# Optimization experiments

Measured on AMD Instinct MI355X. Metric: run time of the kernel, lower is better.

## Reference

```python
import jax, jax.numpy as jnp
import numpy as np

N = 100000   # nodes
E = 1600000  # edges
IN = 128
H = 128
OUT = 128
G = 1000     # graphs


def setup_inputs() -> dict:
    key = jax.random.key(0)
    ks = jax.random.split(key, 6)
    x = jax.random.normal(ks[0], (N, IN), jnp.float32)
    edge_index = jax.random.randint(ks[1], (2, E), 0, N, dtype=jnp.int64)
    batch = jnp.sort(jax.random.randint(ks[2], (N,), 0, G, dtype=jnp.int64))
    # Glorot-ish init for the two GCN linear transforms
    W1 = jax.random.normal(ks[3], (IN, H), jnp.float32) * (1.0 / np.sqrt(IN))
    b1 = jnp.zeros((H,), jnp.float32)
    W2 = jax.random.normal(ks[4], (H, OUT), jnp.float32) * (1.0 / np.sqrt(H))
    b2 = jnp.zeros((OUT,), jnp.float32)
    return {"x": x, "edge_index": edge_index, "batch": batch,
            "W1": W1, "b1": b1, "W2": W2, "b2": b2, "num_graphs": G}


def reference(x, edge_index, batch, W1, b1, W2, b2, num_graphs):
    n = x.shape[0]
    src, dst = edge_index[0], edge_index[1]
    # GCN normalization with self-loops: deg includes the self-loop (+1)
    deg = jax.ops.segment_sum(jnp.ones(src.shape[0], x.dtype), dst,
                              num_segments=n) + 1.0
    dinv = jax.lax.rsqrt(deg)                 # [N]
    norm = dinv[src] * dinv[dst]              # [E] per-edge coefficient
    self_norm = dinv * dinv                   # [N] self-loop coefficient

    def gcn_conv(h, W, b):
        hw = h @ W                                            # [N, F] dense transform
        msg = norm[:, None] * hw[src]                         # gather + scale, [E, F]
        agg = jax.ops.segment_sum(msg, dst, num_segments=n)   # scatter-add
        return agg + self_norm[:, None] * hw + b              # self-loop + bias

    h = jax.nn.relu(gcn_conv(x, W1, b1))
    h = gcn_conv(h, W2, b2)

    # global_mean_pool over graph ids
    sums = jax.ops.segment_sum(h, batch, num_segments=num_graphs)
    counts = jax.ops.segment_sum(jnp.ones(n, h.dtype), batch,
                                 num_segments=num_graphs)
    return sums / jnp.maximum(counts, 1.0)[:, None]
```

## Files before the change

### kernel.cpp

```cpp
#include <hip/hip_runtime.h>
#include <hip/hip_fp16.h>

#define FDIM 128
#define BROWS 64
#define KCH 16
#define NCH (FDIM / KCH)
#define BSHIFT 9
#define BNODES 512
#define EPB 4096


__global__ __launch_bounds__(256) void bucket_count(const int* __restrict__ dst,
                                                    int* __restrict__ bcnt, int E) {
    __shared__ int lc[256];
    lc[threadIdx.x] = 0;
    __syncthreads();
    for (int e = blockIdx.x * blockDim.x + threadIdx.x; e < E;
         e += gridDim.x * blockDim.x)
        atomicAdd(&lc[dst[e] >> BSHIFT], 1);
    __syncthreads();
    int c = lc[threadIdx.x];
    if (c) atomicAdd(&bcnt[threadIdx.x], c);
}

__global__ void bucket_scan(const int* __restrict__ bcnt, int* __restrict__ bbase,
                            int* __restrict__ bcur, int* __restrict__ rp,
                            int E, int n, int nbuck) {
    __shared__ int s[2][256];
    int t = threadIdx.x;
    int v = (t < nbuck) ? bcnt[t] : 0;
    s[0][t] = v;
    __syncthreads();
    int cur = 0;
    for (int off = 1; off < 256; off <<= 1) {
        int x = s[cur][t];
        if (t >= off) x += s[cur][t - off];
        s[cur ^ 1][t] = x;
        cur ^= 1;
        __syncthreads();
    }
    int ex = s[cur][t] - v;
    if (t < nbuck) { bbase[t] = ex; bcur[t] = ex; }
    if (t == 0) { bbase[nbuck] = E; rp[n] = E; }
}

__global__ __launch_bounds__(256) void binscatter(const int* __restrict__ src,
                                                  const int* __restrict__ dst,
                                                  int* __restrict__ bcur,
                                                  int2* __restrict__ eb, int E) {
    __shared__ int lcnt[256];
    __shared__ int gb[256];
    const int t = threadIdx.x;
    const int e0 = blockIdx.x * EPB;
    const int e1 = min(e0 + EPB, E);
    lcnt[t] = 0;
    __syncthreads();
    for (int e = e0 + t; e < e1; e += 256)
        atomicAdd(&lcnt[dst[e] >> BSHIFT], 1);
    __syncthreads();
    int c = lcnt[t];
    if (c) gb[t] = atomicAdd(&bcur[t], c);
    __syncthreads();
    lcnt[t] = 0;
    __syncthreads();
    for (int e = e0 + t; e < e1; e += 256) {
        int d = dst[e];
        int b = d >> BSHIFT;
        int lo = atomicAdd(&lcnt[b], 1);
        eb[gb[b] + lo] = make_int2(src[e], d);
    }
}

__global__ __launch_bounds__(256) void csr_count(const int2* __restrict__ eb,
                                                 const int* __restrict__ bbase,
                                                 int* __restrict__ rp,
                                                 float* __restrict__ dinv, int n) {
    __shared__ int lcnt[BNODES];
    __shared__ int s[2][BNODES];
    const int t = threadIdx.x;
    const int node0 = blockIdx.x << BSHIFT;
    const int nloc = min(BNODES, n - node0);
    lcnt[t] = 0; lcnt[t + 256] = 0;
    __syncthreads();
    const int eb0 = bbase[blockIdx.x], eb1 = bbase[blockIdx.x + 1];
    for (int e = eb0 + t; e < eb1; e += 256)
        atomicAdd(&lcnt[eb[e].y - node0], 1);
    __syncthreads();
    s[0][t] = lcnt[t]; s[0][t + 256] = lcnt[t + 256];
    __syncthreads();
    int cur = 0;
    for (int off = 1; off < BNODES; off <<= 1) {
        int x0 = s[cur][t];       if (t >= off)        x0 += s[cur][t - off];
        int x1 = s[cur][t + 256]; if (t + 256 >= off)  x1 += s[cur][t + 256 - off];
        s[cur ^ 1][t] = x0; s[cur ^ 1][t + 256] = x1;
        cur ^= 1;
        __syncthreads();
    }
    if (t < nloc) {
        rp[node0 + t] = eb0 + s[cur][t] - lcnt[t];
        dinv[node0 + t] = rsqrtf((float)lcnt[t] + 1.0f);
    }
    if (t + 256 < nloc) {
        rp[node0 + t + 256] = eb0 + s[cur][t + 256] - lcnt[t + 256];
        dinv[node0 + t + 256] = rsqrtf((float)lcnt[t + 256] + 1.0f);
    }
}

__global__ __launch_bounds__(256) void csr_fill(const int2* __restrict__ eb,
                                                const int* __restrict__ bbase,
                                                const int* __restrict__ rp,
                                                const float* __restrict__ dinv,
                                                int2* __restrict__ em, int n) {
    __shared__ int lcur[BNODES];
    const int t = threadIdx.x;
    const int node0 = blockIdx.x << BSHIFT;
    const int nloc = min(BNODES, n - node0);
    if (t < nloc) lcur[t] = rp[node0 + t];
    if (t + 256 < nloc) lcur[t + 256] = rp[node0 + t + 256];
    __syncthreads();
    const int eb0 = bbase[blockIdx.x], eb1 = bbase[blockIdx.x + 1];
    for (int e = eb0 + t; e < eb1; e += 256) {
        int2 sd = eb[e];
        int pos = atomicAdd(&lcur[sd.y - node0], 1);
        em[pos] = make_int2(sd.x, __float_as_int(dinv[sd.x] * dinv[sd.y]));
    }
}

__global__ void graph_counts(const int* __restrict__ batch, int* __restrict__ gcnt, int n) {
    int i = blockIdx.x * blockDim.x + threadIdx.x;
    if (i < n) atomicAdd(&gcnt[batch[i]], 1);
}

__global__ __launch_bounds__(256) void gemm128(const float* __restrict__ X,
                                               const float* __restrict__ W,
                                               __half* __restrict__ Y, int n) {
    __shared__ float Ws[FDIM * FDIM];
    __shared__ float xs[2][BROWS][KCH + 4];

    const int tid  = threadIdx.x;
    const int c    = tid & 15;
    const int r    = tid >> 4;
    const int srow = tid >> 2;
    const int skk  = (tid & 3) << 2;
    const int r0   = blockIdx.x * BROWS;

    for (int i = tid; i < FDIM * FDIM; i += 256) Ws[i] = W[i];

    const int grow  = r0 + srow;
    const bool rowok = grow < n;
    const float* xrow = X + (size_t)grow * FDIM + skk;

    float4 v = rowok ? *(const float4*)xrow : float4{0.f, 0.f, 0.f, 0.f};
    *(float4*)&xs[0][srow][skk] = v;
    __syncthreads();

    float accA[4][4], accB[4][4];
#pragma unroll
    for (int m = 0; m < 4; ++m)
#pragma unroll
        for (int i = 0; i < 4; ++i) { accA[m][i] = 0.f; accB[m][i] = 0.f; }

    for (int ch = 0; ch < NCH; ++ch) {
        const int b = ch & 1;
        float4 nv{0.f, 0.f, 0.f, 0.f};
        if (ch + 1 < NCH && rowok)
            nv = *(const float4*)(xrow + (ch + 1) * KCH);
        const int k0 = ch * KCH;
#pragma unroll
        for (int k4 = 0; k4 < KCH; k4 += 4) {
            float4 xv0 = *(const float4*)&xs[b][r][k4];
            float4 xv1 = *(const float4*)&xs[b][r + 16][k4];
            float4 xv2 = *(const float4*)&xs[b][r + 32][k4];
            float4 xv3 = *(const float4*)&xs[b][r + 48][k4];
#define GSTEP(kk, comp)                                                        \
            {                                                                  \
                const float* wp = &Ws[(k0 + k4 + kk) * FDIM + 4 * c];          \
                const float4 w0 = *(const float4*)wp;                          \
                const float4 w1 = *(const float4*)(wp + 64);                   \
                const float xr[4] = {xv0.comp, xv1.comp, xv2.comp, xv3.comp};  \
                _Pragma("unroll")                                              \
                for (int m = 0; m < 4; ++m) {                                  \
                    accA[m][0] = fmaf(xr[m], w0.x, accA[m][0]);                \
                    accA[m][1] = fmaf(xr[m], w0.y, accA[m][1]);                \
                    accA[m][2] = fmaf(xr[m], w0.z, accA[m][2]);                \
                    accB[m][0] = fmaf(xr[m], w1.x, accB[m][0]);                \
                    accB[m][1] = fmaf(xr[m], w1.y, accB[m][1]);                \
                    accB[m][2] = fmaf(xr[m], w1.z, accB[m][2]);                \
                    accB[m][3] = fmaf(xr[m], w1.w, accB[m][3]);                \
                    accA[m][3] = fmaf(xr[m], w0.w, accA[m][3]);                \
                }                                                              \
            }
            GSTEP(0, x) GSTEP(1, y) GSTEP(2, z) GSTEP(3, w)
#undef GSTEP
        }
        if (ch + 1 < NCH)
            *(float4*)&xs[b ^ 1][srow][skk] = nv;
        __syncthreads();
    }

#pragma unroll
    for (int m = 0; m < 4; ++m) {
        int row = r0 + r + 16 * m;
        if (row < n) {
            union { __half2 h[2]; uint2 u; } pa, pb;
            pa.h[0] = __floats2half2_rn(accA[m][0], accA[m][1]);
            pa.h[1] = __floats2half2_rn(accA[m][2], accA[m][3]);
            pb.h[0] = __floats2half2_rn(accB[m][0], accB[m][1]);
            pb.h[1] = __floats2half2_rn(accB[m][2], accB[m][3]);
            *(uint2*)&Y[(size_t)row * FDIM + 4 * c]      = pa.u;
            *(uint2*)&Y[(size_t)row * FDIM + 64 + 4 * c] = pb.u;
        }
    }
}

__device__ __forceinline__ void acc_edge(float4& a, uint2 v, float w) {
    __half2* h = (__half2*)&v;
    float2 f0 = __half22float2(h[0]);
    float2 f1 = __half22float2(h[1]);
    a.x = fmaf(w, f0.x, a.x);
    a.y = fmaf(w, f0.y, a.y);
    a.z = fmaf(w, f1.x, a.z);
    a.w = fmaf(w, f1.y, a.w);
}

__global__ __launch_bounds__(256) void aggregate_relu(
        const __half* __restrict__ hw, const int* __restrict__ rp,
        const int2* __restrict__ em, const float* __restrict__ dinv,
        const float* __restrict__ bias, float* __restrict__ out, int n) {
    const int lane = threadIdx.x & 31;
    const int node = blockIdx.x * 8 + (threadIdx.x >> 5);
    if (node >= n) return;
    const uint2* hw2 = (const uint2*)hw;
    int e0 = rp[node], e1 = rp[node + 1];
    float4 a{0.f, 0.f, 0.f, 0.f};
    int e = e0;
    for (; e + 8 <= e1; e += 8) {
        int2 m[8];
        uint2 v[8];
#pragma unroll
        for (int k = 0; k < 8; ++k) m[k] = em[e + k];
#pragma unroll
        for (int k = 0; k < 8; ++k) v[k] = hw2[(size_t)m[k].x * 32 + lane];
#pragma unroll
        for (int k = 0; k < 8; ++k) acc_edge(a, v[k], __int_as_float(m[k].y));
    }
    for (; e < e1; ++e) {
        int2 m = em[e];
        acc_edge(a, hw2[(size_t)m.x * 32 + lane], __int_as_float(m.y));
    }
    float dv = dinv[node];
    float sn = dv * dv;
    uint2 sv = hw2[(size_t)node * 32 + lane];
    __half2* sh = (__half2*)&sv;
    float2 s0 = __half22float2(sh[0]);
    float2 s1 = __half22float2(sh[1]);
    float4 b = ((const float4*)bias)[lane];
    a.x = fmaxf(fmaf(sn, s0.x, a.x) + b.x, 0.f);
    a.y = fmaxf(fmaf(sn, s0.y, a.y) + b.y, 0.f);
    a.z = fmaxf(fmaf(sn, s1.x, a.z) + b.z, 0.f);
    a.w = fmaxf(fmaf(sn, s1.y, a.w) + b.w, 0.f);
    ((float4*)out)[(size_t)node * 32 + lane] = a;
}

__global__ __launch_bounds__(256) void aggregate_pool(
        const __half* __restrict__ hw, const int* __restrict__ rp,
        const int2* __restrict__ em, const float* __restrict__ dinv,
        const float* __restrict__ bias, const int* __restrict__ batch,
        float* __restrict__ pool, int n) {
    __shared__ float4 part[8][32];
    __shared__ int gs[8];
    const int lane = threadIdx.x & 31;
    const int half = threadIdx.x >> 5;
    const int node = blockIdx.x * 8 + half;
    const bool valid = node < n;
    const uint2* hw2 = (const uint2*)hw;
    int e0 = 0, e1 = 0;
    if (valid) { e0 = rp[node]; e1 = rp[node + 1]; }
    float4 a{0.f, 0.f, 0.f, 0.f};
    int e = e0;
    for (; e + 8 <= e1; e += 8) {
        int2 m[8];
        uint2 v[8];
#pragma unroll
        for (int k = 0; k < 8; ++k) m[k] = em[e + k];
#pragma unroll
        for (int k = 0; k < 8; ++k) v[k] = hw2[(size_t)m[k].x * 32 + lane];
#pragma unroll
        for (int k = 0; k < 8; ++k) acc_edge(a, v[k], __int_as_float(m[k].y));
    }
    for (; e < e1; ++e) {
        int2 m = em[e];
        acc_edge(a, hw2[(size_t)m.x * 32 + lane], __int_as_float(m.y));
    }
    if (valid) {
        float dv = dinv[node];
        float sn = dv * dv;
        uint2 sv = hw2[(size_t)node * 32 + lane];
        __half2* sh = (__half2*)&sv;
        float2 s0 = __half22float2(sh[0]);
        float2 s1 = __half22float2(sh[1]);
        float4 b = ((const float4*)bias)[lane];
        a.x = fmaf(sn, s0.x, a.x) + b.x;
        a.y = fmaf(sn, s0.y, a.y) + b.y;
        a.z = fmaf(sn, s1.x, a.z) + b.z;
        a.w = fmaf(sn, s1.y, a.w) + b.w;
    }
    part[half][lane] = a;
    if (lane == 0) gs[half] = valid ? batch[node] : -1;
    __syncthreads();
    if (half == 0) {
        float4 acc = part[0][lane];
        int g0 = gs[0];
#pragma unroll
        for (int h = 1; h < 8; ++h) {
            if (gs[h] == g0) {
                float4 p = part[h][lane];
                acc.x += p.x; acc.y += p.y; acc.z += p.z; acc.w += p.w;
            } else {
                if (g0 >= 0) {
                    float* dst = &pool[g0 * FDIM + lane * 4];
                    atomicAdd(dst + 0, acc.x); atomicAdd(dst + 1, acc.y);
                    atomicAdd(dst + 2, acc.z); atomicAdd(dst + 3, acc.w);
                }
                g0 = gs[h];
                acc = part[h][lane];
            }
        }
        if (g0 >= 0) {
            float* dst = &pool[g0 * FDIM + lane * 4];
            atomicAdd(dst + 0, acc.x); atomicAdd(dst + 1, acc.y);
            atomicAdd(dst + 2, acc.z); atomicAdd(dst + 3, acc.w);
        }
    }
}

__global__ void pool_div(float* __restrict__ out, const int* __restrict__ gcnt, int total) {
    int i = blockIdx.x * blockDim.x + threadIdx.x;
    if (i < total) {
        int g = i >> 7;
        out[i] /= fmaxf((float)gcnt[g], 1.0f);
    }
}


extern "C" void kernel_launch(void* const* d_in, const int* in_sizes, int n_in,
                              void* d_out, int out_size, void* d_ws, size_t ws_size,
                              hipStream_t stream) {
    const float* x     = (const float*)d_in[0];
    const int*   ei    = (const int*)d_in[1];
    const int*   batch = (const int*)d_in[2];
    const float* W1    = (const float*)d_in[3];
    const float* b1    = (const float*)d_in[4];
    const float* W2    = (const float*)d_in[5];
    const float* b2    = (const float*)d_in[6];
    float* out = (float*)d_out;

    const int N = in_sizes[0] / FDIM;
    const int E = in_sizes[1] / 2;
    const int G = out_size / FDIM;
    const int* src = ei;
    const int* dst = ei + E;
    const int nbuck = (N + BNODES - 1) >> BSHIFT;

    char* p = (char*)d_ws;
    auto alloc = [&](size_t bytes) {
        void* r = (void*)p;
        p += (bytes + 255) & ~(size_t)255;
        return r;
    };
    float*  dinv  = (float*) alloc((size_t)N * 4);
    int*    rp    = (int*)   alloc((size_t)(N + 1) * 4);
    int*    gcnt  = (int*)   alloc((size_t)G * 4);
    int*    bcnt  = (int*)   alloc(256 * 4);
    int*    bbase = (int*)   alloc(257 * 4);
    int*    bcur  = (int*)   alloc(256 * 4);
    int2*   eb    = (int2*)  alloc((size_t)E * 8);
    int2*   em    = (int2*)  alloc((size_t)E * 8);
    __half* hw    = (__half*)alloc((size_t)N * FDIM * 2);
    float*  h1    = (float*) alloc((size_t)N * FDIM * 4);

    hipMemsetAsync(bcnt, 0, 256 * 4, stream);
    hipMemsetAsync(gcnt, 0, (size_t)G * 4, stream);
    hipMemsetAsync(out, 0, (size_t)G * FDIM * 4, stream);

    bucket_count<<<1024, 256, 0, stream>>>(dst, bcnt, E);
    bucket_scan<<<1, 256, 0, stream>>>(bcnt, bbase, bcur, rp, E, N, nbuck);
    binscatter<<<(E + EPB - 1) / EPB, 256, 0, stream>>>(src, dst, bcur, eb, E);
    csr_count<<<nbuck, 256, 0, stream>>>(eb, bbase, rp, dinv, N);
    csr_fill<<<nbuck, 256, 0, stream>>>(eb, bbase, rp, dinv, em, N);
    graph_counts<<<(N + 255) / 256, 256, 0, stream>>>(batch, gcnt, N);

    const int GB = (N + BROWS - 1) / BROWS;
    gemm128<<<GB, 256, 0, stream>>>(x, W1, hw, N);
    aggregate_relu<<<(N + 7) / 8, 256, 0, stream>>>(hw, rp, em, dinv, b1, h1, N);
    gemm128<<<GB, 256, 0, stream>>>(h1, W2, hw, N);
    aggregate_pool<<<(N + 7) / 8, 256, 0, stream>>>(hw, rp, em, dinv, b2, batch, out, N);
    pool_div<<<(G * FDIM + 255) / 256, 256, 0, stream>>>(out, gcnt, G * FDIM);
}
```

Before: 473.4 us.

## Move second GCN linear transform after mean pooling and store h1 in fp16

Uses linearity to reorder the second layer: it aggregates and pools the first-layer activations first, then applies W2 and the bias once per graph in a small pooled GEMM. This removes the full N×128×128 second GEMM and its fp16 intermediate write and read. The relu output h1 is now stored as fp16, which halves its write and its gathered reads but adds rounding error before the second aggregation. The bias is applied only to graphs with nonzero counts, matching mean-pool semantics.

```diff
diff --git a/kernel.cpp b/kernel.cpp
--- a/kernel.cpp
+++ b/kernel.cpp
@@ -226,7 +226,7 @@
 __global__ __launch_bounds__(256) void aggregate_relu(
         const __half* __restrict__ hw, const int* __restrict__ rp,
         const int2* __restrict__ em, const float* __restrict__ dinv,
-        const float* __restrict__ bias, float* __restrict__ out, int n) {
+        const float* __restrict__ bias, __half* __restrict__ out, int n) {
     const int lane = threadIdx.x & 31;
     const int node = blockIdx.x * 8 + (threadIdx.x >> 5);
     if (node >= n) return;
@@ -259,21 +259,23 @@
     a.y = fmaxf(fmaf(sn, s0.y, a.y) + b.y, 0.f);
     a.z = fmaxf(fmaf(sn, s1.x, a.z) + b.z, 0.f);
     a.w = fmaxf(fmaf(sn, s1.y, a.w) + b.w, 0.f);
-    ((float4*)out)[(size_t)node * 32 + lane] = a;
+    union { __half2 h[2]; uint2 u; } pk;
+    pk.h[0] = __floats2half2_rn(a.x, a.y);
+    pk.h[1] = __floats2half2_rn(a.z, a.w);
+    ((uint2*)out)[(size_t)node * 32 + lane] = pk.u;
 }
 
 __global__ __launch_bounds__(256) void aggregate_pool(
-        const __half* __restrict__ hw, const int* __restrict__ rp,
+        const __half* __restrict__ h1, const int* __restrict__ rp,
         const int2* __restrict__ em, const float* __restrict__ dinv,
-        const float* __restrict__ bias, const int* __restrict__ batch,
-        float* __restrict__ pool, int n) {
+        const int* __restrict__ batch, float* __restrict__ pool, int n) {
     __shared__ float4 part[8][32];
     __shared__ int gs[8];
     const int lane = threadIdx.x & 31;
     const int half = threadIdx.x >> 5;
     const int node = blockIdx.x * 8 + half;
     const bool valid = node < n;
-    const uint2* hw2 = (const uint2*)hw;
+    const uint2* hw2 = (const uint2*)h1;
     int e0 = 0, e1 = 0;
     if (valid) { e0 = rp[node]; e1 = rp[node + 1]; }
     float4 a{0.f, 0.f, 0.f, 0.f};
@@ -299,11 +301,10 @@
         __half2* sh = (__half2*)&sv;
         float2 s0 = __half22float2(sh[0]);
         float2 s1 = __half22float2(sh[1]);
-        float4 b = ((const float4*)bias)[lane];
-        a.x = fmaf(sn, s0.x, a.x) + b.x;
-        a.y = fmaf(sn, s0.y, a.y) + b.y;
-        a.z = fmaf(sn, s1.x, a.z) + b.z;
-        a.w = fmaf(sn, s1.y, a.w) + b.w;
+        a.x = fmaf(sn, s0.x, a.x);
+        a.y = fmaf(sn, s0.y, a.y);
+        a.z = fmaf(sn, s1.x, a.z);
+        a.w = fmaf(sn, s1.y, a.w);
     }
     part[half][lane] = a;
     if (lane == 0) gs[half] = valid ? batch[node] : -1;
@@ -334,11 +335,33 @@
     }
 }
 
-__global__ void pool_div(float* __restrict__ out, const int* __restrict__ gcnt, int total) {
-    int i = blockIdx.x * blockDim.x + threadIdx.x;
-    if (i < total) {
-        int g = i >> 7;
-        out[i] /= fmaxf((float)gcnt[g], 1.0f);
+__global__ __launch_bounds__(256) void pool_gemm(const float* __restrict__ pool,
+                                                 const int* __restrict__ gcnt,
+                                                 const float* __restrict__ W2,
+                                                 const float* __restrict__ b2,
+                                                 float* __restrict__ out, int G) {
+    __shared__ float Ws[FDIM * FDIM];
+    __shared__ float row[2][FDIM];
+    for (int i = threadIdx.x; i < FDIM * FDIM; i += 256) Ws[i] = W2[i];
+    const int j  = threadIdx.x & 127;
+    const int gh = threadIdx.x >> 7;
+    for (int g0 = blockIdx.x * 2; g0 < G; g0 += gridDim.x * 2) {
+        const int g = g0 + gh;
+        __syncthreads();
+        int c = 0;
+        if (g < G) {
+            c = gcnt[g];
+            float inv = (c > 0) ? 1.0f / (float)c : 0.0f;
+            row[gh][j] = pool[g * FDIM + j] * inv;
+        }
+        __syncthreads();
+        if (g < G) {
+            float acc = (c > 0) ? b2[j] : 0.0f;
+#pragma unroll
+            for (int k = 0; k < FDIM; ++k)
+                acc = fmaf(row[gh][k], Ws[k * FDIM + j], acc);
+            out[g * FDIM + j] = acc;
+        }
     }
 }
 
@@ -377,11 +400,12 @@
     int2*   eb    = (int2*)  alloc((size_t)E * 8);
     int2*   em    = (int2*)  alloc((size_t)E * 8);
     __half* hw    = (__half*)alloc((size_t)N * FDIM * 2);
-    float*  h1    = (float*) alloc((size_t)N * FDIM * 4);
+    __half* h1    = (__half*)alloc((size_t)N * FDIM * 2);
+    float*  pool  = (float*) alloc((size_t)G * FDIM * 4);
 
     hipMemsetAsync(bcnt, 0, 256 * 4, stream);
     hipMemsetAsync(gcnt, 0, (size_t)G * 4, stream);
-    hipMemsetAsync(out, 0, (size_t)G * FDIM * 4, stream);
+    hipMemsetAsync(pool, 0, (size_t)G * FDIM * 4, stream);
 
     bucket_count<<<1024, 256, 0, stream>>>(dst, bcnt, E);
     bucket_scan<<<1, 256, 0, stream>>>(bcnt, bbase, bcur, rp, E, N, nbuck);
@@ -393,7 +417,6 @@
     const int GB = (N + BROWS - 1) / BROWS;
     gemm128<<<GB, 256, 0, stream>>>(x, W1, hw, N);
     aggregate_relu<<<(N + 7) / 8, 256, 0, stream>>>(hw, rp, em, dinv, b1, h1, N);
-    gemm128<<<GB, 256, 0, stream>>>(h1, W2, hw, N);
-    aggregate_pool<<<(N + 7) / 8, 256, 0, stream>>>(hw, rp, em, dinv, b2, batch, out, N);
-    pool_div<<<(G * FDIM + 255) / 256, 256, 0, stream>>>(out, gcnt, G * FDIM);
-}
+    aggregate_pool<<<(N + 7) / 8, 256, 0, stream>>>(h1, rp, em, dinv, batch, pool, N);
+    pool_gemm<<<64, 256, 0, stream>>>(pool, gcnt, W2, b2, out, G);
+}
```

After: 433.7 us. -8.4%, faster.
